# Kernel optimization log

Hardware: AMD Instinct MI355X
Metric: run time of the kernel (lower is better)

## Reference

```python
import jax, jax.numpy as jnp
import numpy as np

B, S = 32, 8192
HE, HD = 256, 256  # encoder_hidden_size, decoder_hidden_size


def setup_inputs() -> dict:
    key = jax.random.key(0)
    ks = jax.random.split(key, 8)
    scale = 1.0 / np.sqrt(HD)
    scale_e = 1.0 / np.sqrt(HE)
    return {
        "query": jax.random.normal(ks[0], (B, 1, HD), dtype=jnp.float32),
        "keys": jax.random.normal(ks[1], (B, S, HE), dtype=jnp.float32),
        "Wa_w": jax.random.uniform(ks[2], (HD, HD), jnp.float32, -scale, scale),
        "Wa_b": jax.random.uniform(ks[3], (HD,), jnp.float32, -scale, scale),
        "Ua_w": jax.random.uniform(ks[4], (HD, HE), jnp.float32, -scale_e, scale_e),
        "Ua_b": jax.random.uniform(ks[5], (HD,), jnp.float32, -scale_e, scale_e),
        "Va_w": jax.random.uniform(ks[6], (1, HD), jnp.float32, -scale, scale),
        "Va_b": jax.random.uniform(ks[7], (1,), jnp.float32, -scale, scale),
    }


def reference(query, keys, Wa_w, Wa_b, Ua_w, Ua_b, Va_w, Va_b):
    # q_proj: [B, 1, HD]; k_proj: [B, S, HD]
    q_proj = jnp.einsum("bqd,hd->bqh", query, Wa_w) + Wa_b
    k_proj = jnp.einsum("bse,he->bsh", keys, Ua_w) + Ua_b
    # scores: [B, S] -> [B, 1, S]
    scores = jnp.einsum("bsh,h->bs", jnp.tanh(q_proj + k_proj), Va_w[0]) + Va_b[0]
    weights = jax.nn.softmax(scores, axis=-1)[:, None, :]  # [B, 1, S]
    context = jnp.einsum("bqs,bse->bqe", weights, keys)    # [B, 1, HE]
    return (context, weights)
```

## Files before the change

### kernel.cpp

```cpp
#include <hip/hip_runtime.h>
#include <hip/hip_bf16.h>
#include <stdint.h>

#define B_ 32
#define S_ 8192
#define HD_ 256
#define HE_ 256
#define CHUNK 256
#define ROWS 16
#define MSTEPS (CHUNK/ROWS)
#define NCHUNK (S_/CHUNK)

typedef __attribute__((ext_vector_type(8))) short bf16x8;
typedef __attribute__((ext_vector_type(4))) float f32x4;

__device__ __forceinline__ uint32_t cvt_pk_bf16(float lo, float hi) {
  uint32_t r;
  asm("v_cvt_pk_bf16_f32 %0, %1, %2" : "=v"(r) : "v"(lo), "v"(hi));
  return r;
}
__device__ __forceinline__ float bf2f(unsigned short h) {
  return __uint_as_float(((uint32_t)h) << 16);
}
__device__ __forceinline__ float tanh_fast(float x) {
  float e = __expf(2.0f * x);
  return 1.0f - 2.0f * __builtin_amdgcn_rcpf(e + 1.0f);
}
template<int CTRL>
__device__ __forceinline__ float dpp_shr_add(float v) {
  int t = __builtin_amdgcn_update_dpp(0, __float_as_int(v), CTRL, 0xf, 0xf, true);
  return v + __int_as_float(t);
}
__device__ __forceinline__ float row16_sum(float v) {
  v = dpp_shr_add<0x118>(v);
  v = dpp_shr_add<0x114>(v);
  v = dpp_shr_add<0x112>(v);
  v = dpp_shr_add<0x111>(v);
  return v;
}

__global__ void prep_kernel(const float* __restrict__ query,
                            const float* __restrict__ Wa_w,
                            const float* __restrict__ Wa_b,
                            const float* __restrict__ Ua_w,
                            const float* __restrict__ Ua_b,
                            float* __restrict__ qv,
                            unsigned short* __restrict__ ua_bf) {
  const int blk = blockIdx.x, t = threadIdx.x;
  if (blk < B_) {
    __shared__ float qs[HD_];
    qs[t] = query[blk * HD_ + t];
    __syncthreads();
    const float* wr = Wa_w + (size_t)t * HD_;
    float s = Wa_b[t] + Ua_b[t];
#pragma unroll 8
    for (int d = 0; d < HD_; ++d) s += qs[d] * wr[d];
    qv[blk * HD_ + t] = s;
  } else {
    const int base = (blk - B_) * 2048 + t * 8;
    float4 v0 = *(const float4*)(Ua_w + base);
    float4 v1 = *(const float4*)(Ua_w + base + 4);
    uint4 pk;
    pk.x = cvt_pk_bf16(v0.x, v0.y);
    pk.y = cvt_pk_bf16(v0.z, v0.w);
    pk.z = cvt_pk_bf16(v1.x, v1.y);
    pk.w = cvt_pk_bf16(v1.z, v1.w);
    *(uint4*)(ua_bf + base) = pk;
  }
}

__global__ __launch_bounds__(256, 2)
void main_kernel(const float* __restrict__ keys,
                 const float* __restrict__ qv,
                 const float* __restrict__ Va_w,
                 const unsigned short* __restrict__ ua_bf,
                 float* __restrict__ wexp_g,
                 float* __restrict__ partials) {
  __shared__ __align__(16) char kt[2 * ROWS * 512];
  __shared__ float sc_sum[2][16];
  __shared__ __align__(16) float num_l[4][64][4];

  const int t = threadIdx.x;
  const int b = blockIdx.y;
  const int chunk = blockIdx.x;
  const int s0 = chunk * CHUNK;
  const int lane = t & 63;
  const int w = t >> 6;
  const int ln = lane & 15;
  const int hi = lane >> 4;

  const unsigned short* ub = ua_bf + (size_t)(w * 64 + ln) * HE_ + hi * 8;
  bf16x8 bb0[8], bb1[8], bb2[8], bb3[8];
#pragma unroll
  for (int k = 0; k < 8; ++k) {
    bb0[k] = *(const bf16x8*)(ub + k * 32);
    bb1[k] = *(const bf16x8*)(ub + 16 * HE_ + k * 32);
    bb2[k] = *(const bf16x8*)(ub + 32 * HE_ + k * 32);
    bb3[k] = *(const bf16x8*)(ub + 48 * HE_ + k * 32);
  }
  const int hbase = b * HD_ + w * 64 + ln;
  const float q0  = qv[hbase];
  const float q1  = qv[hbase + 16];
  const float q2  = qv[hbase + 32];
  const float q3  = qv[hbase + 48];
  const float va0 = Va_w[w * 64 + ln];
  const float va1 = Va_w[w * 64 + 16 + ln];
  const float va2 = Va_w[w * 64 + 32 + ln];
  const float va3 = Va_w[w * 64 + 48 + ln];

  const int srow = t >> 5;
  const int scch = t & 31;
  const float* ksrcA = keys + ((size_t)b * S_ + s0 + srow) * HE_ + scch * 8;
  const float* ksrcB = ksrcA + 8 * HE_;
  const int ldsoffA = srow * 512 + ((scch * 16) ^ ((srow & 7) << 4));
  const int ldsoffB = ldsoffA + 8 * 512;

  if (t < 32) ((float*)sc_sum)[t] = 0.f;
  {
    float4 a0 = *(const float4*)(ksrcA);
    float4 a1 = *(const float4*)(ksrcA + 4);
    float4 c0 = *(const float4*)(ksrcB);
    float4 c1 = *(const float4*)(ksrcB + 4);
    uint4 pk;
    pk.x = cvt_pk_bf16(a0.x, a0.y);
    pk.y = cvt_pk_bf16(a0.z, a0.w);
    pk.z = cvt_pk_bf16(a1.x, a1.y);
    pk.w = cvt_pk_bf16(a1.z, a1.w);
    *(uint4*)(kt + ldsoffA) = pk;
    pk.x = cvt_pk_bf16(c0.x, c0.y);
    pk.y = cvt_pk_bf16(c0.z, c0.w);
    pk.z = cvt_pk_bf16(c1.x, c1.y);
    pk.w = cvt_pk_bf16(c1.z, c1.w);
    *(uint4*)(kt + ldsoffB) = pk;
  }
  __syncthreads();

  const int asw = (ln & 7) << 4;
  float num4[4] = {0.f, 0.f, 0.f, 0.f};

  for (int i = 0; i < MSTEPS; ++i) {
    char* cur = kt + (i & 1) * (ROWS * 512);
    char* nxt = kt + ((i + 1) & 1) * (ROWS * 512);

    float4 ga0, ga1, gc0, gc1;
    if (i + 1 < MSTEPS) {
      const float* kA = ksrcA + (size_t)(i + 1) * ROWS * HE_;
      const float* kB = ksrcB + (size_t)(i + 1) * ROWS * HE_;
      ga0 = *(const float4*)(kA);
      ga1 = *(const float4*)(kA + 4);
      gc0 = *(const float4*)(kB);
      gc1 = *(const float4*)(kB + 4);
    }

    f32x4 a0 = {0.f,0.f,0.f,0.f}, a1 = {0.f,0.f,0.f,0.f};
    f32x4 a2 = {0.f,0.f,0.f,0.f}, a3 = {0.f,0.f,0.f,0.f};
    const char* arow = cur + ln * 512;
#pragma unroll
    for (int k = 0; k < 8; ++k) {
      bf16x8 af = *(const bf16x8*)(arow + ((k * 64 + hi * 16) ^ asw));
      a0 = __builtin_amdgcn_mfma_f32_16x16x32_bf16(af, bb0[k], a0, 0, 0, 0);
      a1 = __builtin_amdgcn_mfma_f32_16x16x32_bf16(af, bb1[k], a1, 0, 0, 0);
      a2 = __builtin_amdgcn_mfma_f32_16x16x32_bf16(af, bb2[k], a2, 0, 0, 0);
      a3 = __builtin_amdgcn_mfma_f32_16x16x32_bf16(af, bb3[k], a3, 0, 0, 0);
    }

#pragma unroll
    for (int r = 0; r < 4; ++r) {
      float v = tanh_fast(a0[r] + q0) * va0 + tanh_fast(a1[r] + q1) * va1
              + tanh_fast(a2[r] + q2) * va2 + tanh_fast(a3[r] + q3) * va3;
      v = row16_sum(v);
      if (ln == 15) atomicAdd(&sc_sum[i & 1][hi * 4 + r], v);
    }
    __syncthreads();

    const float e0 = __expf(sc_sum[i & 1][4 * w + 0]);
    const float e1 = __expf(sc_sum[i & 1][4 * w + 1]);
    const float e2 = __expf(sc_sum[i & 1][4 * w + 2]);
    const float e3 = __expf(sc_sum[i & 1][4 * w + 3]);
    if (lane == 0) {
      float* wg = wexp_g + (size_t)b * S_ + s0 + i * ROWS + 4 * w;
      wg[0] = e0; wg[1] = e1; wg[2] = e2; wg[3] = e3;
    }
    if (t < 16) sc_sum[(i + 1) & 1][t] = 0.f;

#pragma unroll
    for (int j = 0; j < 4; ++j) {
      const int row = 4 * w + j;
      const float e = (j == 0) ? e0 : (j == 1) ? e1 : (j == 2) ? e2 : e3;
      uint2 kv = *(const uint2*)(cur + row * 512 + ((lane * 8) ^ ((row & 7) << 4)));
      num4[0] += e * bf2f((unsigned short)(kv.x & 0xffff));
      num4[1] += e * bf2f((unsigned short)(kv.x >> 16));
      num4[2] += e * bf2f((unsigned short)(kv.y & 0xffff));
      num4[3] += e * bf2f((unsigned short)(kv.y >> 16));
    }

    if (i + 1 < MSTEPS) {
      uint4 pk;
      pk.x = cvt_pk_bf16(ga0.x, ga0.y);
      pk.y = cvt_pk_bf16(ga0.z, ga0.w);
      pk.z = cvt_pk_bf16(ga1.x, ga1.y);
      pk.w = cvt_pk_bf16(ga1.z, ga1.w);
      *(uint4*)(nxt + ldsoffA) = pk;
      pk.x = cvt_pk_bf16(gc0.x, gc0.y);
      pk.y = cvt_pk_bf16(gc0.z, gc0.w);
      pk.z = cvt_pk_bf16(gc1.x, gc1.y);
      pk.w = cvt_pk_bf16(gc1.z, gc1.w);
      *(uint4*)(nxt + ldsoffB) = pk;
    }
    __syncthreads();
  }

  *(float4*)&num_l[w][lane][0] = make_float4(num4[0], num4[1], num4[2], num4[3]);
  __syncthreads();
  {
    float s = 0.f;
#pragma unroll
    for (int ww = 0; ww < 4; ++ww) s += num_l[ww][t >> 2][t & 3];
    partials[((size_t)b * NCHUNK + chunk) * 256 + t] = s;
  }
}

__global__ void combine_kernel(const float* __restrict__ wexp_g,
                               const float* __restrict__ partials,
                               float* __restrict__ out) {
  __shared__ float red[4];
  __shared__ float rdsh;
  const int b = blockIdx.x, t = threadIdx.x;
  const float* we = wexp_g + (size_t)b * S_;
  float s = 0.f;
#pragma unroll 4
  for (int i = t; i < S_; i += 256) s += we[i];
#pragma unroll
  for (int mm = 32; mm; mm >>= 1) s += __shfl_xor(s, mm, 64);
  if ((t & 63) == 0) red[t >> 6] = s;
  __syncthreads();
  if (t == 0) rdsh = 1.0f / (red[0] + red[1] + red[2] + red[3]);
  __syncthreads();
  const float rd = rdsh;

  const float* pb = partials + (size_t)b * NCHUNK * 256;
  float num = 0.f;
#pragma unroll 4
  for (int i = 0; i < NCHUNK; ++i) num += pb[i * 256 + t];
  out[b * HE_ + t] = num * rd;

  float* wout = out + B_ * HE_ + (size_t)b * S_;
#pragma unroll 4
  for (int i = t; i < S_; i += 256) wout[i] = we[i] * rd;
}

extern "C" void kernel_launch(void* const* d_in, const int* in_sizes, int n_in,
                              void* d_out, int out_size, void* d_ws, size_t ws_size,
                              hipStream_t stream) {
  const float* query = (const float*)d_in[0];
  const float* keys  = (const float*)d_in[1];
  const float* Wa_w  = (const float*)d_in[2];
  const float* Wa_b  = (const float*)d_in[3];
  const float* Ua_w  = (const float*)d_in[4];
  const float* Ua_b  = (const float*)d_in[5];
  const float* Va_w  = (const float*)d_in[6];
  float* out = (float*)d_out;

  char* ws = (char*)d_ws;
  float* qv             = (float*)ws;
  unsigned short* ua_bf = (unsigned short*)(ws + 32 * 1024);
  float* wexp_g         = (float*)(ws + 160 * 1024);
  float* partials       = (float*)(ws + 160 * 1024 + 1048576);

  prep_kernel<<<64, 256, 0, stream>>>(query, Wa_w, Wa_b, Ua_w, Ua_b, qv, ua_bf);
  dim3 g(NCHUNK, B_);
  main_kernel<<<g, 256, 0, stream>>>(keys, qv, Va_w, ua_bf, wexp_g, partials);
  combine_kernel<<<B_, 256, 0, stream>>>(wexp_g, partials, out);
}
```

Baseline: 85.30 us.

## Deepen key prefetch to two tiles and defer context accumulation by one step

```diff
diff --git a/kernel.cpp b/kernel.cpp
--- a/kernel.cpp
+++ b/kernel.cpp
@@ -10,6 +10,7 @@
 #define ROWS 16
 #define MSTEPS (CHUNK/ROWS)
 #define NCHUNK (S_/CHUNK)
+#define TILE (ROWS * 512)
 
 typedef __attribute__((ext_vector_type(8))) short bf16x8;
 typedef __attribute__((ext_vector_type(4))) float f32x4;
@@ -76,8 +77,8 @@
                  const unsigned short* __restrict__ ua_bf,
                  float* __restrict__ wexp_g,
                  float* __restrict__ partials) {
-  __shared__ __align__(16) char kt[2 * ROWS * 512];
-  __shared__ float sc_sum[2][16];
+  __shared__ __align__(16) char kt[4 * TILE];
+  __shared__ float sc3[3][16];
   __shared__ __align__(16) float num_l[4][64][4];
 
   const int t = threadIdx.x;
@@ -115,41 +116,47 @@
   const int ldsoffA = srow * 512 + ((scch * 16) ^ ((srow & 7) << 4));
   const int ldsoffB = ldsoffA + 8 * 512;
 
-  if (t < 32) ((float*)sc_sum)[t] = 0.f;
-  {
-    float4 a0 = *(const float4*)(ksrcA);
-    float4 a1 = *(const float4*)(ksrcA + 4);
-    float4 c0 = *(const float4*)(ksrcB);
-    float4 c1 = *(const float4*)(ksrcB + 4);
+  float4 gA[4], gB[4];
+
+  auto issue = [&](float4* g, int tl) {
+    const float* kA = ksrcA + (size_t)tl * ROWS * HE_;
+    const float* kB = ksrcB + (size_t)tl * ROWS * HE_;
+    g[0] = *(const float4*)(kA);
+    g[1] = *(const float4*)(kA + 4);
+    g[2] = *(const float4*)(kB);
+    g[3] = *(const float4*)(kB + 4);
+  };
+  auto stagew = [&](const float4* g, char* dst) {
     uint4 pk;
-    pk.x = cvt_pk_bf16(a0.x, a0.y);
-    pk.y = cvt_pk_bf16(a0.z, a0.w);
-    pk.z = cvt_pk_bf16(a1.x, a1.y);
-    pk.w = cvt_pk_bf16(a1.z, a1.w);
-    *(uint4*)(kt + ldsoffA) = pk;
-    pk.x = cvt_pk_bf16(c0.x, c0.y);
-    pk.y = cvt_pk_bf16(c0.z, c0.w);
-    pk.z = cvt_pk_bf16(c1.x, c1.y);
-    pk.w = cvt_pk_bf16(c1.z, c1.w);
-    *(uint4*)(kt + ldsoffB) = pk;
-  }
+    pk.x = cvt_pk_bf16(g[0].x, g[0].y);
+    pk.y = cvt_pk_bf16(g[0].z, g[0].w);
+    pk.z = cvt_pk_bf16(g[1].x, g[1].y);
+    pk.w = cvt_pk_bf16(g[1].z, g[1].w);
+    *(uint4*)(dst + ldsoffA) = pk;
+    pk.x = cvt_pk_bf16(g[2].x, g[2].y);
+    pk.y = cvt_pk_bf16(g[2].z, g[2].w);
+    pk.z = cvt_pk_bf16(g[3].x, g[3].y);
+    pk.w = cvt_pk_bf16(g[3].z, g[3].w);
+    *(uint4*)(dst + ldsoffB) = pk;
+  };
+
+  if (t < 48) ((float*)sc3)[t] = 0.f;
+  issue(gA, 0);
+  stagew(gA, kt);
+  issue(gB, 1);
   __syncthreads();
 
   const int asw = (ln & 7) << 4;
   float num4[4] = {0.f, 0.f, 0.f, 0.f};
 
+#pragma unroll
   for (int i = 0; i < MSTEPS; ++i) {
-    char* cur = kt + (i & 1) * (ROWS * 512);
-    char* nxt = kt + ((i + 1) & 1) * (ROWS * 512);
-
-    float4 ga0, ga1, gc0, gc1;
-    if (i + 1 < MSTEPS) {
-      const float* kA = ksrcA + (size_t)(i + 1) * ROWS * HE_;
-      const float* kB = ksrcB + (size_t)(i + 1) * ROWS * HE_;
-      ga0 = *(const float4*)(kA);
-      ga1 = *(const float4*)(kA + 4);
-      gc0 = *(const float4*)(kB);
-      gc1 = *(const float4*)(kB + 4);
+    char* cur = kt + (i % 4) * TILE;
+    char* stg = kt + ((i + 1) % 4) * TILE;
+    char* prv = kt + ((i + 3) % 4) * TILE;
+
+    if (i + 2 < MSTEPS) {
+      if (i & 1) issue(gB, i + 2); else issue(gA, i + 2);
     }
 
     f32x4 a0 = {0.f,0.f,0.f,0.f}, a1 = {0.f,0.f,0.f,0.f};
@@ -164,50 +171,65 @@
       a3 = __builtin_amdgcn_mfma_f32_16x16x32_bf16(af, bb3[k], a3, 0, 0, 0);
     }
 
+    if (i > 0) {
+      const float* scp = sc3[(i + 2) % 3];
+      const float e0 = __expf(scp[4 * w + 0]);
+      const float e1 = __expf(scp[4 * w + 1]);
+      const float e2 = __expf(scp[4 * w + 2]);
+      const float e3 = __expf(scp[4 * w + 3]);
+      if (lane == 0) {
+        float* wg = wexp_g + (size_t)b * S_ + s0 + (i - 1) * ROWS + 4 * w;
+        wg[0] = e0; wg[1] = e1; wg[2] = e2; wg[3] = e3;
+      }
+#pragma unroll
+      for (int j = 0; j < 4; ++j) {
+        const int row = 4 * w + j;
+        const float e = (j == 0) ? e0 : (j == 1) ? e1 : (j == 2) ? e2 : e3;
+        uint2 kv = *(const uint2*)(prv + row * 512 + ((lane * 8) ^ ((row & 7) << 4)));
+        num4[0] += e * bf2f((unsigned short)(kv.x & 0xffff));
+        num4[1] += e * bf2f((unsigned short)(kv.x >> 16));
+        num4[2] += e * bf2f((unsigned short)(kv.y & 0xffff));
+        num4[3] += e * bf2f((unsigned short)(kv.y >> 16));
+      }
+    }
+
 #pragma unroll
     for (int r = 0; r < 4; ++r) {
       float v = tanh_fast(a0[r] + q0) * va0 + tanh_fast(a1[r] + q1) * va1
               + tanh_fast(a2[r] + q2) * va2 + tanh_fast(a3[r] + q3) * va3;
       v = row16_sum(v);
-      if (ln == 15) atomicAdd(&sc_sum[i & 1][hi * 4 + r], v);
+      if (ln == 15) atomicAdd(&sc3[i % 3][hi * 4 + r], v);
+    }
+
+    if (t < 16) sc3[(i + 1) % 3][t] = 0.f;
+
+    if (i + 1 < MSTEPS) {
+      if ((i + 1) & 1) stagew(gB, stg); else stagew(gA, stg);
     }
     __syncthreads();
-
-    const float e0 = __expf(sc_sum[i & 1][4 * w + 0]);
-    const float e1 = __expf(sc_sum[i & 1][4 * w + 1]);
-    const float e2 = __expf(sc_sum[i & 1][4 * w + 2]);
-    const float e3 = __expf(sc_sum[i & 1][4 * w + 3]);
+  }
+
+  {
+    const float* scp = sc3[(MSTEPS - 1) % 3];
+    const char* prv = kt + ((MSTEPS - 1) % 4) * TILE;
+    const float e0 = __expf(scp[4 * w + 0]);
+    const float e1 = __expf(scp[4 * w + 1]);
+    const float e2 = __expf(scp[4 * w + 2]);
+    const float e3 = __expf(scp[4 * w + 3]);
     if (lane == 0) {
-      float* wg = wexp_g + (size_t)b * S_ + s0 + i * ROWS + 4 * w;
+      float* wg = wexp_g + (size_t)b * S_ + s0 + (MSTEPS - 1) * ROWS + 4 * w;
       wg[0] = e0; wg[1] = e1; wg[2] = e2; wg[3] = e3;
     }
-    if (t < 16) sc_sum[(i + 1) & 1][t] = 0.f;
-
 #pragma unroll
     for (int j = 0; j < 4; ++j) {
       const int row = 4 * w + j;
       const float e = (j == 0) ? e0 : (j == 1) ? e1 : (j == 2) ? e2 : e3;
-      uint2 kv = *(const uint2*)(cur + row * 512 + ((lane * 8) ^ ((row & 7) << 4)));
+      uint2 kv = *(const uint2*)(prv + row * 512 + ((lane * 8) ^ ((row & 7) << 4)));
       num4[0] += e * bf2f((unsigned short)(kv.x & 0xffff));
       num4[1] += e * bf2f((unsigned short)(kv.x >> 16));
       num4[2] += e * bf2f((unsigned short)(kv.y & 0xffff));
       num4[3] += e * bf2f((unsigned short)(kv.y >> 16));
     }
-
-    if (i + 1 < MSTEPS) {
-      uint4 pk;
-      pk.x = cvt_pk_bf16(ga0.x, ga0.y);
-      pk.y = cvt_pk_bf16(ga0.z, ga0.w);
-      pk.z = cvt_pk_bf16(ga1.x, ga1.y);
-      pk.w = cvt_pk_bf16(ga1.z, ga1.w);
-      *(uint4*)(nxt + ldsoffA) = pk;
-      pk.x = cvt_pk_bf16(gc0.x, gc0.y);
-      pk.y = cvt_pk_bf16(gc0.z, gc0.w);
-      pk.z = cvt_pk_bf16(gc1.x, gc1.y);
-      pk.w = cvt_pk_bf16(gc1.z, gc1.w);
-      *(uint4*)(nxt + ldsoffB) = pk;
-    }
-    __syncthreads();
   }
 
   *(float4*)&num_l[w][lane][0] = make_float4(num4[0], num4[1], num4[2], num4[3]);
```

Result: slower. 144.3 us (+69.2%).
